# Kernel optimization log

Measured on AMD Instinct MI355X. Metric: run time of the kernel, lower is better.

The kernel has to match this reference:

```python
import jax, jax.numpy as jnp
import numpy as np

LP, LQ, B, D = 4096, 4096, 32, 512  # lp, lq, batch, hidden (=in_size1=in_size2)
WSCALE = 0.04  # ~ torch Linear default uniform bound 1/sqrt(512)


def setup_inputs() -> dict:
    key = jax.random.key(0)
    ks = jax.random.split(key, 11)
    return {
        "h": jax.random.normal(ks[0], (LP, B, D), jnp.float32),
        "u": jax.random.normal(ks[1], (B, LQ, D), jnp.float32),
        "v": jax.random.normal(ks[2], (B, D, 1), jnp.float32),
        "Wu_w": jax.random.normal(ks[3], (D, D), jnp.float32) * WSCALE,
        "Wu_b": jax.random.normal(ks[4], (D,), jnp.float32) * WSCALE,
        "Wh_w": jax.random.normal(ks[5], (D, D), jnp.float32) * WSCALE,
        "Wha_w": jax.random.normal(ks[6], (D, D), jnp.float32) * WSCALE,
        "W_ih": jax.random.normal(ks[7], (3 * D, D), jnp.float32) * WSCALE,
        "W_hh": jax.random.normal(ks[8], (3 * D, D), jnp.float32) * WSCALE,
        "b_ih": jax.random.normal(ks[9], (3 * D,), jnp.float32) * WSCALE,
        "b_hh": jax.random.normal(ks[10], (3 * D,), jnp.float32) * WSCALE,
    }


def _gru_cell(x, hprev, W_ih, W_hh, b_ih, b_hh):
    # torch GRUCell semantics
    gi = x @ W_ih.T + b_ih          # [B, 3D]
    gh = hprev @ W_hh.T + b_hh      # [B, 3D]
    i_r, i_z, i_n = jnp.split(gi, 3, axis=-1)
    h_r, h_z, h_n = jnp.split(gh, 3, axis=-1)
    r = jax.nn.sigmoid(i_r + h_r)
    z = jax.nn.sigmoid(i_z + h_z)
    n = jnp.tanh(i_n + r * h_n)
    return (1.0 - z) * n + z * hprev


def reference(h, u, v, Wu_w, Wu_b, Wh_w, Wha_w, W_ih, W_hh, b_ih, b_hh):
    # h: [lp, B, d1], u: [B, lq, d2], v: [B, H, 1]
    vb = v[:, :, 0]  # [B, H]
    # --- attention over u ---
    xq = jnp.tanh(jnp.einsum('bqd,hd->bqh', u, Wu_w) + Wu_b)   # [B, lq, H]
    s = jnp.einsum('bqh,bh->bq', xq, vb)                        # bmm(x, v).squeeze
    a = jax.nn.softmax(s, axis=1)
    r = jnp.einsum('bq,bqd->bd', a, u)                          # [B, d2]
    # --- attention over h conditioned on r, twice with GRU update in between ---
    Whh_proj = jnp.einsum('pbd,hd->pbh', h, Wh_w)               # [lp, B, H] (reused)

    def h_attn(rvec):
        x = jnp.tanh(Whh_proj + (rvec @ Wha_w.T)[None])         # [lp, B, H]
        s = jnp.einsum('pbh,bh->bp', x, vb)                     # [B, lp]
        return jax.nn.softmax(s, axis=1)

    p1 = h_attn(r)
    c = jnp.einsum('bp,pbd->bd', p1, h)                         # [B, d1]
    r2 = _gru_cell(c, r, W_ih, W_hh, b_ih, b_hh)                # [B, d2]
    p2 = h_attn(r2)
    return (p1, p2)
```

## Files before the change

kernel.cpp:

```cpp
#include <hip/hip_runtime.h>
#include <hip/hip_bf16.h>

typedef __attribute__((ext_vector_type(4))) float f4;
typedef __attribute__((ext_vector_type(8))) _Float16 h8;
typedef __attribute__((ext_vector_type(4))) _Float16 h4;

#define MTOT 131072

__device__ __forceinline__ float fast_tanh(float x){
    float e = exp2f(x * 2.8853900817779268f);
    return 1.0f - 2.0f * __builtin_amdgcn_rcpf(e + 1.0f);
}
__device__ __forceinline__ float fast_sigmoid(float x){
    return __builtin_amdgcn_rcpf(1.0f + exp2f(-x * 1.4426950408889634f));
}
__device__ __forceinline__ float wave_reduce_sum(float v){
    #pragma unroll
    for (int off = 32; off; off >>= 1) v += __shfl_down(v, off, 64);
    return v;
}

__device__ __forceinline__ void gl_lds16(const void* g, void* l){
    __builtin_amdgcn_global_load_lds(
        (const __attribute__((address_space(1))) void*)g,
        (__attribute__((address_space(3))) void*)l, 16, 0, 0);
}

__global__ __launch_bounds__(256) void k_pack_w(const float* __restrict__ W, _Float16* __restrict__ Wp){
    const int idx = blockIdx.x * 4 + (threadIdx.x >> 6);
    const int l = threadIdx.x & 63;
    const int n = (idx >> 4) * 16 + (l & 15);
    const int k = (idx & 15) * 32 + (l >> 4) * 8;
    const float* src = W + n * 512 + k;
    f4 s0 = *(const f4*)(src);
    f4 s1 = *(const f4*)(src + 4);
    h8 v;
    #pragma unroll
    for (int i = 0; i < 4; i++){ v[i] = (_Float16)s0[i]; v[4+i] = (_Float16)s1[i]; }
    *(h8*)(Wp + (idx << 9) + l * 8) = v;
}

union SMem {
    struct { float A[2][4096]; _Float16 W[2][8192]; } st;
    _Float16 ep[64][264];
};

template<int MODE>
__global__ __launch_bounds__(512) void k_score_gemm(
    const float* __restrict__ A,
    const _Float16* __restrict__ Wp,
    const float* __restrict__ vb,
    const float* __restrict__ addvec,
    float* __restrict__ spart,
    _Float16* __restrict__ whh)
{
    __shared__ __align__(16) SMem sm;

    const int tid  = threadIdx.x;
    const int lane = tid & 63;
    const int wv   = tid >> 6;
    const int wr   = wv >> 2;
    const int wc   = wv & 3;
    const int mt   = blockIdx.x >> 1;
    const int nc   = blockIdx.x & 1;
    const int m0   = mt * 128;
    const int n0   = nc * 256;

    const int lr = lane & 15;
    const int kq = lane >> 4;

    const int arow0 = tid >> 3;
    const int aseg  = tid & 7;

    auto stage = [&](int kt, int buf){
        #pragma unroll
        for (int i = 0; i < 2; i++){
            const int row = arow0 + i*64;
            const int sg  = aseg ^ (row & 7);
            const float* g = A + (long)(m0 + row)*512 + kt*32 + sg*4;
            char* l = (char*)&sm.st.A[0][0] + buf*16384 + (i*512 + wv*64)*16;
            gl_lds16(g, l);
        }
        #pragma unroll
        for (int i = 0; i < 2; i++){
            const int chunk = i*8 + wv;
            const _Float16* g = Wp + ((long)((nc*16 + chunk)*16 + kt))*512 + lane*8;
            char* l = (char*)&sm.st.W[0][0] + buf*16384 + chunk*1024;
            gl_lds16(g, l);
        }
    };

    f4 acc[4][4] = {};

    stage(0, 0);
    __syncthreads();

    const int plo = (2*kq)     ^ (lr & 7);
    const int phi = (2*kq + 1) ^ (lr & 7);

    for (int kt = 0; kt < 16; ++kt){
        const int buf = kt & 1;
        if (kt < 15) stage(kt + 1, buf ^ 1);

        const float* Ab = &sm.st.A[0][0] + buf*4096;
        h8 af[4];
        #pragma unroll
        for (int mi = 0; mi < 4; mi++){
            const int row = wr*64 + mi*16 + lr;
            f4 lo = *(const f4*)(Ab + row*32 + plo*4);
            f4 hi = *(const f4*)(Ab + row*32 + phi*4);
            h8 v;
            #pragma unroll
            for (int i = 0; i < 4; i++){ v[i] = (_Float16)lo[i]; v[4+i] = (_Float16)hi[i]; }
            af[mi] = v;
        }
        const _Float16* Wb = &sm.st.W[0][0] + buf*8192;
        h8 bf[4];
        #pragma unroll
        for (int ni = 0; ni < 4; ni++)
            bf[ni] = *(const h8*)(Wb + (wc*4 + ni)*512 + lane*8);

        #pragma unroll
        for (int mi = 0; mi < 4; mi++)
            #pragma unroll
            for (int ni = 0; ni < 4; ni++)
                acc[mi][ni] = __builtin_amdgcn_mfma_f32_16x16x32_f16(af[mi], bf[ni], acc[mi][ni], 0, 0, 0);

        __syncthreads();
    }

    const int jrow = (lane >> 4) * 4;
    for (int hf = 0; hf < 2; ++hf){
        if (wr == hf){
            #pragma unroll
            for (int mi = 0; mi < 4; mi++)
                #pragma unroll
                for (int ni = 0; ni < 4; ni++)
                    #pragma unroll
                    for (int j = 0; j < 4; j++)
                        sm.ep[mi*16 + jrow + j][wc*64 + ni*16 + lr] = (_Float16)acc[mi][ni][j];
        }
        __syncthreads();

        if (MODE == 1 && whh){
            const int row = tid >> 3, seg = tid & 7;
            const int m = m0 + hf*64 + row;
            const _Float16* esrc = &sm.ep[row][seg*32];
            _Float16* gdst = whh + (long)m*512 + n0 + seg*32;
            #pragma unroll
            for (int i = 0; i < 4; i++)
                *(h8*)(gdst + i*8) = *(const h8*)(esrc + i*8);
        }

        #pragma unroll
        for (int rr = 0; rr < 8; ++rr){
            const int erow = wv*8 + rr;
            const int m = m0 + hf*64 + erow;
            const int b = (MODE == 0) ? (m >> 12) : (m & 31);
            const int n = n0 + lane*4;
            h4 hv = *(const h4*)&sm.ep[erow][lane*4];
            f4 vbv = *(const f4*)&vb[b*512 + n];
            f4 adv;
            if (MODE == 0) adv = *(const f4*)&addvec[n];
            else           adv = *(const f4*)&addvec[b*512 + n];
            float p = 0.f;
            #pragma unroll
            for (int i = 0; i < 4; i++)
                p += fast_tanh((float)hv[i] + adv[i]) * vbv[i];
            p = wave_reduce_sum(p);
            if (lane == 0){
                const int sIdx = (MODE == 0) ? m : (((m & 31) << 12) | (m >> 5));
                spart[nc*MTOT + sIdx] = p;
            }
        }
        __syncthreads();
    }
}

__global__ __launch_bounds__(256) void k_softmax(const float* __restrict__ s0,
        const float* __restrict__ s1, float* __restrict__ out)
{
    __shared__ float red[8];
    __shared__ float bcast[2];
    const int b = blockIdx.x, t = threadIdx.x;
    const int wv = t >> 6, lane = t & 63;
    const float* p0 = s0 + b*4096;
    const float* p1 = s1 ? s1 + b*4096 : nullptr;
    float vals[16];
    float mx = -3.0e38f;
    #pragma unroll
    for (int i = 0; i < 16; i++){
        float v = p0[t + i*256];
        if (p1) v += p1[t + i*256];
        vals[i] = v;
        mx = fmaxf(mx, v);
    }
    #pragma unroll
    for (int off = 32; off; off >>= 1) mx = fmaxf(mx, __shfl_down(mx, off, 64));
    if (lane == 0) red[wv] = mx;
    __syncthreads();
    if (t == 0) bcast[0] = fmaxf(fmaxf(red[0], red[1]), fmaxf(red[2], red[3]));
    __syncthreads();
    const float gmax = bcast[0];
    float sum = 0.f;
    #pragma unroll
    for (int i = 0; i < 16; i++){
        vals[i] = exp2f((vals[i] - gmax) * 1.4426950408889634f);
        sum += vals[i];
    }
    sum = wave_reduce_sum(sum);
    if (lane == 0) red[wv] = sum;
    __syncthreads();
    if (t == 0) bcast[1] = red[0] + red[1] + red[2] + red[3];
    __syncthreads();
    const float inv = 1.0f / bcast[1];
    #pragma unroll
    for (int i = 0; i < 16; i++) out[b*4096 + t + i*256] = vals[i] * inv;
}

__global__ __launch_bounds__(512) void k_weighted_rowsum(
    const float* __restrict__ wts, const float* __restrict__ X,
    float* __restrict__ part, int mode)
{
    const int b = blockIdx.x, ch = blockIdx.y, d = threadIdx.x;
    float acc = 0.f;
    const int q0 = ch * 256;
    for (int q = q0; q < q0 + 256; ++q){
        const float w = wts[b*4096 + q];
        if (fabsf(w) > 1e-20f){
            const float* xp = (mode == 0) ? (X + ((long)(b*4096 + q) * 512) + d)
                                          : (X + ((long)(q*32 + b) * 512) + d);
            acc += w * xp[0];
        }
    }
    part[(ch*32 + b)*512 + d] = acc;
}

__global__ void k_reduce_part(const float* __restrict__ part, float* __restrict__ out){
    const int b = blockIdx.x, d = threadIdx.x;
    float s = 0.f;
    #pragma unroll
    for (int ch = 0; ch < 16; ++ch) s += part[(ch*32 + b)*512 + d];
    out[b*512 + d] = s;
}

__global__ __launch_bounds__(256) void k_matvec(
    const float* __restrict__ W, const float* __restrict__ x,
    const float* __restrict__ bias, float* __restrict__ out, int N)
{
    __shared__ float xs[512];
    const int b = blockIdx.x, t = threadIdx.x;
    xs[t] = x[b*512 + t];
    xs[t + 256] = x[b*512 + 256 + t];
    __syncthreads();
    const int wv = t >> 6, lane = t & 63;
    const int rbase = blockIdx.y*32 + wv*8;
    for (int rr = 0; rr < 8; ++rr){
        const int row = rbase + rr;
        const float* wp = W + (long)row*512;
        float p = 0.f;
        #pragma unroll
        for (int j = 0; j < 8; j++) p += wp[lane + j*64] * xs[lane + j*64];
        p = wave_reduce_sum(p);
        if (lane == 0) out[b*N + row] = p + (bias ? bias[row] : 0.f);
    }
}

__global__ void k_gru(const float* __restrict__ gi, const float* __restrict__ gh,
                      const float* __restrict__ r, float* __restrict__ r2)
{
    const int b = blockIdx.x, d = threadIdx.x;
    const float* gib = gi + b*1536;
    const float* ghb = gh + b*1536;
    const float rg = fast_sigmoid(gib[d]        + ghb[d]);
    const float z  = fast_sigmoid(gib[512 + d]  + ghb[512 + d]);
    const float n  = fast_tanh   (gib[1024 + d] + rg * ghb[1024 + d]);
    r2[b*512 + d] = (1.f - z)*n + z*r[b*512 + d];
}

__global__ __launch_bounds__(256) void k_t2(const _Float16* __restrict__ whh,
        const float* __restrict__ vb, const float* __restrict__ ra2, float* __restrict__ t2)
{
    const int wv = threadIdx.x >> 6, lane = threadIdx.x & 63;
    const int mbase = blockIdx.x*32 + wv*8;
    for (int rr = 0; rr < 8; ++rr){
        const int m = mbase + rr;
        const int b = m & 31;
        h8 hv = *(const h8*)(whh + (long)m*512 + lane*8);
        const float* rp  = ra2 + b*512 + lane*8;
        const float* vbp = vb  + b*512 + lane*8;
        float p = 0.f;
        #pragma unroll
        for (int i = 0; i < 8; i++)
            p += fast_tanh((float)hv[i] + rp[i]) * vbp[i];
        p = wave_reduce_sum(p);
        if (lane == 0) t2[((m & 31) << 12) | (m >> 5)] = p;
    }
}

extern "C" void kernel_launch(void* const* d_in, const int* in_sizes, int n_in,
                              void* d_out, int out_size, void* d_ws, size_t ws_size,
                              hipStream_t stream)
{
    const float* h_    = (const float*)d_in[0];
    const float* u_    = (const float*)d_in[1];
    const float* vb    = (const float*)d_in[2];
    const float* Wu_w  = (const float*)d_in[3];
    const float* Wu_b  = (const float*)d_in[4];
    const float* Wh_w  = (const float*)d_in[5];
    const float* Wha_w = (const float*)d_in[6];
    const float* W_ih  = (const float*)d_in[7];
    const float* W_hh  = (const float*)d_in[8];
    const float* b_ih  = (const float*)d_in[9];
    const float* b_hh  = (const float*)d_in[10];
    float* out = (float*)d_out;

    char* ws = (char*)d_ws;
    float*    spart = (float*)(ws + 0);
    float*    tpart = (float*)(ws + 1048576);
    float*    a_    = (float*)(ws + 2097152);
    _Float16* Wpu   = (_Float16*)(ws + 2621440);
    _Float16* Wph   = (_Float16*)(ws + 3145728);
    float*    r_    = (float*)(ws + 3670016);
    float*    ra1   = (float*)(ws + 3735552);
    float*    c_    = (float*)(ws + 3801088);
    float*    r2    = (float*)(ws + 3866624);
    float*    ra2   = (float*)(ws + 3932160);
    float*    gi    = (float*)(ws + 3997696);
    float*    gh    = (float*)(ws + 4194304);
    float*    rpart = (float*)(ws + 4390912);
    float*    cpart = (float*)(ws + 5439488);
    _Float16* whh   = (_Float16*)(ws + 8388608);
    const bool big = ws_size >= (size_t)8388608 + (size_t)MTOT * 512 * 2;

    k_pack_w<<<128, 256, 0, stream>>>(Wu_w, Wpu);
    k_pack_w<<<128, 256, 0, stream>>>(Wh_w, Wph);

    k_score_gemm<0><<<2048, 512, 0, stream>>>(u_, Wpu, vb, Wu_b, spart, nullptr);
    k_softmax<<<32, 256, 0, stream>>>(spart, spart + MTOT, a_);
    k_weighted_rowsum<<<dim3(32, 16), 512, 0, stream>>>(a_, u_, rpart, 0);
    k_reduce_part<<<32, 512, 0, stream>>>(rpart, r_);
    k_matvec<<<dim3(32, 16), 256, 0, stream>>>(Wha_w, r_, nullptr, ra1, 512);

    k_score_gemm<1><<<2048, 512, 0, stream>>>(h_, Wph, vb, ra1, tpart, big ? whh : nullptr);
    k_softmax<<<32, 256, 0, stream>>>(tpart, tpart + MTOT, out);

    k_weighted_rowsum<<<dim3(32, 16), 512, 0, stream>>>(out, h_, cpart, 1);
    k_reduce_part<<<32, 512, 0, stream>>>(cpart, c_);
    k_matvec<<<dim3(32, 48), 256, 0, stream>>>(W_ih, c_, b_ih, gi, 1536);
    k_matvec<<<dim3(32, 48), 256, 0, stream>>>(W_hh, r_, b_hh, gh, 1536);
    k_gru<<<32, 512, 0, stream>>>(gi, gh, r_, r2);
    k_matvec<<<dim3(32, 16), 256, 0, stream>>>(Wha_w, r2, nullptr, ra2, 512);

    if (big){
        k_t2<<<4096, 256, 0, stream>>>(whh, vb, ra2, tpart);
        k_softmax<<<32, 256, 0, stream>>>(tpart, nullptr, out + MTOT);
    } else {
        k_score_gemm<2><<<2048, 512, 0, stream>>>(h_, Wph, vb, ra2, tpart, nullptr);
        k_softmax<<<32, 256, 0, stream>>>(tpart, tpart + MTOT, out + MTOT);
    }
}
```

Baseline: 598.8 us.

## Triple-buffer score GEMM and fuse softmax/rowsum/matvec/GRU tails into per-batch kernels

The score GEMM moves from a double-buffered to a triple-buffered global-to-LDS pipeline. It uses explicit vmcnt waits, raw barriers and raised MFMA priority, so loads for step kt+3 overlap compute. The softmax, weighted rowsum, partial reduce, matvec and GRU kernels are replaced by two fused kernels with one block per batch. Each builds a sparse list of non-negligible weights and does the rowsum and matvecs in-block, and the two weight-pack launches are merged into one. This cuts about ten launches and intermediate buffers, but the rowsum and matvecs now run on only 32 blocks, which could underuse the GPU.

Measured after the change: 919.6 us. 1.54x slower.

```diff
diff --git a/kernel.cpp b/kernel.cpp
--- a/kernel.cpp
+++ b/kernel.cpp
@@ -26,8 +26,14 @@
         (__attribute__((address_space(3))) void*)l, 16, 0, 0);
 }
 
-__global__ __launch_bounds__(256) void k_pack_w(const float* __restrict__ W, _Float16* __restrict__ Wp){
-    const int idx = blockIdx.x * 4 + (threadIdx.x >> 6);
+__global__ __launch_bounds__(256) void k_pack_both(
+    const float* __restrict__ Wu, const float* __restrict__ Wh,
+    _Float16* __restrict__ Pu, _Float16* __restrict__ Ph)
+{
+    const int g = blockIdx.x;
+    const float* W = (g < 128) ? Wu : Wh;
+    _Float16*    P = (g < 128) ? Pu : Ph;
+    const int idx = (g & 127) * 4 + (threadIdx.x >> 6);
     const int l = threadIdx.x & 63;
     const int n = (idx >> 4) * 16 + (l & 15);
     const int k = (idx & 15) * 32 + (l >> 4) * 8;
@@ -37,11 +43,11 @@
     h8 v;
     #pragma unroll
     for (int i = 0; i < 4; i++){ v[i] = (_Float16)s0[i]; v[4+i] = (_Float16)s1[i]; }
-    *(h8*)(Wp + (idx << 9) + l * 8) = v;
+    *(h8*)(P + (idx << 9) + l * 8) = v;
 }
 
 union SMem {
-    struct { float A[2][4096]; _Float16 W[2][8192]; } st;
+    struct { float A[3][4096]; _Float16 W[3][8192]; } st;
     _Float16 ep[64][264];
 };
 
@@ -92,15 +98,20 @@
 
     f4 acc[4][4] = {};
 
-    stage(0, 0);
-    __syncthreads();
+    stage(0, 0); stage(1, 1); stage(2, 2);
+    __builtin_amdgcn_sched_barrier(0);
 
     const int plo = (2*kq)     ^ (lr & 7);
     const int phi = (2*kq + 1) ^ (lr & 7);
 
+    #pragma unroll
     for (int kt = 0; kt < 16; ++kt){
-        const int buf = kt & 1;
-        if (kt < 15) stage(kt + 1, buf ^ 1);
+        const int buf = kt % 3;
+        if (kt < 14)       asm volatile("s_waitcnt vmcnt(8)" ::: "memory");
+        else if (kt == 14) asm volatile("s_waitcnt vmcnt(4)" ::: "memory");
+        else               asm volatile("s_waitcnt vmcnt(0)" ::: "memory");
+        __builtin_amdgcn_s_barrier();
+        __builtin_amdgcn_sched_barrier(0);
 
         const float* Ab = &sm.st.A[0][0] + buf*4096;
         h8 af[4];
@@ -120,14 +131,23 @@
         for (int ni = 0; ni < 4; ni++)
             bf[ni] = *(const h8*)(Wb + (wc*4 + ni)*512 + lane*8);
 
+        asm volatile("s_waitcnt lgkmcnt(0)" ::: "memory");
+        __builtin_amdgcn_sched_barrier(0);
+        __builtin_amdgcn_s_barrier();
+        __builtin_amdgcn_sched_barrier(0);
+
+        if (kt < 13) stage(kt + 3, buf);
+
+        __builtin_amdgcn_s_setprio(1);
         #pragma unroll
         for (int mi = 0; mi < 4; mi++)
             #pragma unroll
             for (int ni = 0; ni < 4; ni++)
                 acc[mi][ni] = __builtin_amdgcn_mfma_f32_16x16x32_f16(af[mi], bf[ni], acc[mi][ni], 0, 0, 0);
-
-        __syncthreads();
-    }
+        __builtin_amdgcn_s_setprio(0);
+    }
+    __builtin_amdgcn_sched_barrier(0);
+    __syncthreads();
 
     const int jrow = (lane >> 4) * 4;
     for (int hf = 0; hf < 2; ++hf){
@@ -177,6 +197,163 @@
     }
 }
 
+__global__ __launch_bounds__(512) void k_fused1(
+    const float* __restrict__ sp, const float* __restrict__ u,
+    const float* __restrict__ Wha,
+    float* __restrict__ r_out, float* __restrict__ ra1)
+{
+    __shared__ float aw[4096];
+    __shared__ int   qlist[4096];
+    __shared__ float xl[512];
+    __shared__ float red[8];
+    __shared__ float bc[2];
+    __shared__ int   cnt;
+    const int b = blockIdx.x, t = threadIdx.x;
+    const int wv = t >> 6, lane = t & 63;
+    if (t == 0) cnt = 0;
+    const float* p0 = sp + b*4096;
+    const float* p1 = sp + MTOT + b*4096;
+    float v[8]; float mx = -3.0e38f;
+    #pragma unroll
+    for (int i = 0; i < 8; i++){
+        v[i] = p0[t + i*512] + p1[t + i*512];
+        mx = fmaxf(mx, v[i]);
+    }
+    #pragma unroll
+    for (int off = 32; off; off >>= 1) mx = fmaxf(mx, __shfl_down(mx, off, 64));
+    if (lane == 0) red[wv] = mx;
+    __syncthreads();
+    if (t == 0){ float m2 = red[0]; for (int i = 1; i < 8; i++) m2 = fmaxf(m2, red[i]); bc[0] = m2; }
+    __syncthreads();
+    const float gmax = bc[0];
+    float sum = 0.f;
+    #pragma unroll
+    for (int i = 0; i < 8; i++){
+        float e = exp2f((v[i] - gmax) * 1.4426950408889634f);
+        v[i] = e; aw[t + i*512] = e; sum += e;
+        if (e > 1e-16f){ int idx = atomicAdd(&cnt, 1); qlist[idx] = t + i*512; }
+    }
+    sum = wave_reduce_sum(sum);
+    if (lane == 0) red[wv] = sum;
+    __syncthreads();
+    if (t == 0){ float s2 = 0.f; for (int i = 0; i < 8; i++) s2 += red[i]; bc[1] = s2; }
+    __syncthreads();
+    const float inv = 1.0f / bc[1];
+    const int n = cnt;
+    float acc = 0.f;
+    for (int i = 0; i < n; i++){
+        const int q = qlist[i];
+        acc += aw[q] * u[((long)(b*4096 + q))*512 + t];
+    }
+    acc *= inv;
+    xl[t] = acc;
+    r_out[b*512 + t] = acc;
+    __syncthreads();
+    for (int j = 0; j < 64; j++){
+        const int row = wv*64 + j;
+        const float* wp = Wha + (long)row*512;
+        float p = 0.f;
+        #pragma unroll
+        for (int jj = 0; jj < 8; jj++) p += wp[lane + jj*64] * xl[lane + jj*64];
+        p = wave_reduce_sum(p);
+        if (lane == 0) ra1[b*512 + row] = p;
+    }
+}
+
+__global__ __launch_bounds__(512) void k_fused2(
+    const float* __restrict__ tp, const float* __restrict__ h,
+    const float* __restrict__ r_in,
+    const float* __restrict__ Wih, const float* __restrict__ Whh_,
+    const float* __restrict__ bih, const float* __restrict__ bhh,
+    const float* __restrict__ Wha,
+    float* __restrict__ p1_out, float* __restrict__ ra2)
+{
+    __shared__ float aw[4096];
+    __shared__ int   qlist[4096];
+    __shared__ float cl[512], rl[512], r2l[512];
+    __shared__ float gl[1536], hl[1536];
+    __shared__ float red[8];
+    __shared__ float bc[2];
+    __shared__ int   cnt;
+    const int b = blockIdx.x, t = threadIdx.x;
+    const int wv = t >> 6, lane = t & 63;
+    if (t == 0) cnt = 0;
+    rl[t] = r_in[b*512 + t];
+    const float* p0 = tp + b*4096;
+    const float* p1 = tp + MTOT + b*4096;
+    float v[8]; float mx = -3.0e38f;
+    #pragma unroll
+    for (int i = 0; i < 8; i++){
+        v[i] = p0[t + i*512] + p1[t + i*512];
+        mx = fmaxf(mx, v[i]);
+    }
+    #pragma unroll
+    for (int off = 32; off; off >>= 1) mx = fmaxf(mx, __shfl_down(mx, off, 64));
+    if (lane == 0) red[wv] = mx;
+    __syncthreads();
+    if (t == 0){ float m2 = red[0]; for (int i = 1; i < 8; i++) m2 = fmaxf(m2, red[i]); bc[0] = m2; }
+    __syncthreads();
+    const float gmax = bc[0];
+    float sum = 0.f;
+    #pragma unroll
+    for (int i = 0; i < 8; i++){
+        float e = exp2f((v[i] - gmax) * 1.4426950408889634f);
+        v[i] = e; aw[t + i*512] = e; sum += e;
+        if (e > 1e-16f){ int idx = atomicAdd(&cnt, 1); qlist[idx] = t + i*512; }
+    }
+    sum = wave_reduce_sum(sum);
+    if (lane == 0) red[wv] = sum;
+    __syncthreads();
+    if (t == 0){ float s2 = 0.f; for (int i = 0; i < 8; i++) s2 += red[i]; bc[1] = s2; }
+    __syncthreads();
+    const float inv = 1.0f / bc[1];
+    const int n = cnt;
+    #pragma unroll
+    for (int i = 0; i < 8; i++) p1_out[b*4096 + t + i*512] = v[i] * inv;
+    float acc = 0.f;
+    for (int i = 0; i < n; i++){
+        const int q = qlist[i];
+        acc += aw[q] * h[((long)(q*32 + b))*512 + t];
+    }
+    cl[t] = acc * inv;
+    __syncthreads();
+    for (int j = 0; j < 192; j++){
+        const int row = wv*192 + j;
+        const float* wp = Wih + (long)row*512;
+        float p = 0.f;
+        #pragma unroll
+        for (int jj = 0; jj < 8; jj++) p += wp[lane + jj*64] * cl[lane + jj*64];
+        p = wave_reduce_sum(p);
+        if (lane == 0) gl[row] = p + bih[row];
+    }
+    for (int j = 0; j < 192; j++){
+        const int row = wv*192 + j;
+        const float* wp = Whh_ + (long)row*512;
+        float p = 0.f;
+        #pragma unroll
+        for (int jj = 0; jj < 8; jj++) p += wp[lane + jj*64] * rl[lane + jj*64];
+        p = wave_reduce_sum(p);
+        if (lane == 0) hl[row] = p + bhh[row];
+    }
+    __syncthreads();
+    {
+        const float rg = fast_sigmoid(gl[t] + hl[t]);
+        const float z  = fast_sigmoid(gl[512 + t] + hl[512 + t]);
+        const float nn = fast_tanh(gl[1024 + t] + rg * hl[1024 + t]);
+        r2l[t] = (1.f - z)*nn + z*rl[t];
+    }
+    __syncthreads();
+    for (int j = 0; j < 64; j++){
+        const int row = wv*64 + j;
+        const float* wp = Wha + (long)row*512;
+        float p = 0.f;
+        #pragma unroll
+        for (int jj = 0; jj < 8; jj++) p += wp[lane + jj*64] * r2l[lane + jj*64];
+        p = wave_reduce_sum(p);
+        if (lane == 0) ra2[b*512 + row] = p;
+    }
+}
+
 __global__ __launch_bounds__(256) void k_softmax(const float* __restrict__ s0,
         const float* __restrict__ s1, float* __restrict__ out)
 {
@@ -216,66 +393,6 @@
     const float inv = 1.0f / bcast[1];
     #pragma unroll
     for (int i = 0; i < 16; i++) out[b*4096 + t + i*256] = vals[i] * inv;
-}
-
-__global__ __launch_bounds__(512) void k_weighted_rowsum(
-    const float* __restrict__ wts, const float* __restrict__ X,
-    float* __restrict__ part, int mode)
-{
-    const int b = blockIdx.x, ch = blockIdx.y, d = threadIdx.x;
-    float acc = 0.f;
-    const int q0 = ch * 256;
-    for (int q = q0; q < q0 + 256; ++q){
-        const float w = wts[b*4096 + q];
-        if (fabsf(w) > 1e-20f){
-            const float* xp = (mode == 0) ? (X + ((long)(b*4096 + q) * 512) + d)
-                                          : (X + ((long)(q*32 + b) * 512) + d);
-            acc += w * xp[0];
-        }
-    }
-    part[(ch*32 + b)*512 + d] = acc;
-}
-
-__global__ void k_reduce_part(const float* __restrict__ part, float* __restrict__ out){
-    const int b = blockIdx.x, d = threadIdx.x;
-    float s = 0.f;
-    #pragma unroll
-    for (int ch = 0; ch < 16; ++ch) s += part[(ch*32 + b)*512 + d];
-    out[b*512 + d] = s;
-}
-
-__global__ __launch_bounds__(256) void k_matvec(
-    const float* __restrict__ W, const float* __restrict__ x,
-    const float* __restrict__ bias, float* __restrict__ out, int N)
-{
-    __shared__ float xs[512];
-    const int b = blockIdx.x, t = threadIdx.x;
-    xs[t] = x[b*512 + t];
-    xs[t + 256] = x[b*512 + 256 + t];
-    __syncthreads();
-    const int wv = t >> 6, lane = t & 63;
-    const int rbase = blockIdx.y*32 + wv*8;
-    for (int rr = 0; rr < 8; ++rr){
-        const int row = rbase + rr;
-        const float* wp = W + (long)row*512;
-        float p = 0.f;
-        #pragma unroll
-        for (int j = 0; j < 8; j++) p += wp[lane + j*64] * xs[lane + j*64];
-        p = wave_reduce_sum(p);
-        if (lane == 0) out[b*N + row] = p + (bias ? bias[row] : 0.f);
-    }
-}
-
-__global__ void k_gru(const float* __restrict__ gi, const float* __restrict__ gh,
-                      const float* __restrict__ r, float* __restrict__ r2)
-{
-    const int b = blockIdx.x, d = threadIdx.x;
-    const float* gib = gi + b*1536;
-    const float* ghb = gh + b*1536;
-    const float rg = fast_sigmoid(gib[d]        + ghb[d]);
-    const float z  = fast_sigmoid(gib[512 + d]  + ghb[512 + d]);
-    const float n  = fast_tanh   (gib[1024 + d] + rg * ghb[1024 + d]);
-    r2[b*512 + d] = (1.f - z)*n + z*r[b*512 + d];
 }
 
 __global__ __launch_bounds__(256) void k_t2(const _Float16* __restrict__ whh,
@@ -318,39 +435,21 @@
     char* ws = (char*)d_ws;
     float*    spart = (float*)(ws + 0);
     float*    tpart = (float*)(ws + 1048576);
-    float*    a_    = (float*)(ws + 2097152);
     _Float16* Wpu   = (_Float16*)(ws + 2621440);
     _Float16* Wph   = (_Float16*)(ws + 3145728);
     float*    r_    = (float*)(ws + 3670016);
     float*    ra1   = (float*)(ws + 3735552);
-    float*    c_    = (float*)(ws + 3801088);
-    float*    r2    = (float*)(ws + 3866624);
     float*    ra2   = (float*)(ws + 3932160);
-    float*    gi    = (float*)(ws + 3997696);
-    float*    gh    = (float*)(ws + 4194304);
-    float*    rpart = (float*)(ws + 4390912);
-    float*    cpart = (float*)(ws + 5439488);
     _Float16* whh   = (_Float16*)(ws + 8388608);
     const bool big = ws_size >= (size_t)8388608 + (size_t)MTOT * 512 * 2;
 
-    k_pack_w<<<128, 256, 0, stream>>>(Wu_w, Wpu);
-    k_pack_w<<<128, 256, 0, stream>>>(Wh_w, Wph);
+    k_pack_both<<<256, 256, 0, stream>>>(Wu_w, Wh_w, Wpu, Wph);
 
     k_score_gemm<0><<<2048, 512, 0, stream>>>(u_, Wpu, vb, Wu_b, spart, nullptr);
-    k_softmax<<<32, 256, 0, stream>>>(spart, spart + MTOT, a_);
-    k_weighted_rowsum<<<dim3(32, 16), 512, 0, stream>>>(a_, u_, rpart, 0);
-    k_reduce_part<<<32, 512, 0, stream>>>(rpart, r_);
-    k_matvec<<<dim3(32, 16), 256, 0, stream>>>(Wha_w, r_, nullptr, ra1, 512);
+    k_fused1<<<32, 512, 0, stream>>>(spart, u_, Wha_w, r_, ra1);
 
     k_score_gemm<1><<<2048, 512, 0, stream>>>(h_, Wph, vb, ra1, tpart, big ? whh : nullptr);
-    k_softmax<<<32, 256, 0, stream>>>(tpart, tpart + MTOT, out);
-
-    k_weighted_rowsum<<<dim3(32, 16), 512, 0, stream>>>(out, h_, cpart, 1);
-    k_reduce_part<<<32, 512, 0, stream>>>(cpart, c_);
-    k_matvec<<<dim3(32, 48), 256, 0, stream>>>(W_ih, c_, b_ih, gi, 1536);
-    k_matvec<<<dim3(32, 48), 256, 0, stream>>>(W_hh, r_, b_hh, gh, 1536);
-    k_gru<<<32, 512, 0, stream>>>(gi, gh, r_, r2);
-    k_matvec<<<dim3(32, 16), 256, 0, stream>>>(Wha_w, r2, nullptr, ra2, 512);
+    k_fused2<<<32, 512, 0, stream>>>(tpart, h_, r_, W_ih, W_hh, b_ih, b_hh, Wha_w, out, ra2);
 
     if (big){
         k_t2<<<4096, 256, 0, stream>>>(whh, vb, ra2, tpart);
```

## Triple-buffer score GEMM pipeline, merge weight packing, widen rowsum split, vectorize matvec

Applied to the files above, without the earlier changes.

The score GEMM moves from a double-buffered to a triple-buffered LDS pipeline. It waits with explicit vmcnt and uses raw barriers, setprio around the MFMAs, and a fully unrolled k loop, so global loads for the stage after next overlap compute. The two weight-pack launches are merged into one, and the weighted row-sum is split into 32 chunks instead of 16 for more parallelism, with one shared partial buffer. The matvec now uses contiguous float4 loads per lane. The larger LDS footprint may lower occupancy, and the partial buffer grows to 2 MB in the workspace.

Result: no change. 593.0 us (-1.0%).

```diff
diff --git a/kernel.cpp b/kernel.cpp
--- a/kernel.cpp
+++ b/kernel.cpp
@@ -26,8 +26,14 @@
         (__attribute__((address_space(3))) void*)l, 16, 0, 0);
 }
 
-__global__ __launch_bounds__(256) void k_pack_w(const float* __restrict__ W, _Float16* __restrict__ Wp){
-    const int idx = blockIdx.x * 4 + (threadIdx.x >> 6);
+__global__ __launch_bounds__(256) void k_pack_both(
+    const float* __restrict__ Wu, const float* __restrict__ Wh,
+    _Float16* __restrict__ Pu, _Float16* __restrict__ Ph)
+{
+    const int g = blockIdx.x;
+    const float* W = (g < 128) ? Wu : Wh;
+    _Float16*    P = (g < 128) ? Pu : Ph;
+    const int idx = (g & 127) * 4 + (threadIdx.x >> 6);
     const int l = threadIdx.x & 63;
     const int n = (idx >> 4) * 16 + (l & 15);
     const int k = (idx & 15) * 32 + (l >> 4) * 8;
@@ -37,11 +43,11 @@
     h8 v;
     #pragma unroll
     for (int i = 0; i < 4; i++){ v[i] = (_Float16)s0[i]; v[4+i] = (_Float16)s1[i]; }
-    *(h8*)(Wp + (idx << 9) + l * 8) = v;
+    *(h8*)(P + (idx << 9) + l * 8) = v;
 }
 
 union SMem {
-    struct { float A[2][4096]; _Float16 W[2][8192]; } st;
+    struct { float A[3][4096]; _Float16 W[3][8192]; } st;
     _Float16 ep[64][264];
 };
 
@@ -92,15 +98,20 @@
 
     f4 acc[4][4] = {};
 
-    stage(0, 0);
-    __syncthreads();
+    stage(0, 0); stage(1, 1); stage(2, 2);
+    __builtin_amdgcn_sched_barrier(0);
 
     const int plo = (2*kq)     ^ (lr & 7);
     const int phi = (2*kq + 1) ^ (lr & 7);
 
+    #pragma unroll
     for (int kt = 0; kt < 16; ++kt){
-        const int buf = kt & 1;
-        if (kt < 15) stage(kt + 1, buf ^ 1);
+        const int buf = kt % 3;
+        if (kt < 14)       asm volatile("s_waitcnt vmcnt(8)" ::: "memory");
+        else if (kt == 14) asm volatile("s_waitcnt vmcnt(4)" ::: "memory");
+        else               asm volatile("s_waitcnt vmcnt(0)" ::: "memory");
+        __builtin_amdgcn_s_barrier();
+        __builtin_amdgcn_sched_barrier(0);
 
         const float* Ab = &sm.st.A[0][0] + buf*4096;
         h8 af[4];
@@ -120,14 +131,23 @@
         for (int ni = 0; ni < 4; ni++)
             bf[ni] = *(const h8*)(Wb + (wc*4 + ni)*512 + lane*8);
 
+        asm volatile("s_waitcnt lgkmcnt(0)" ::: "memory");
+        __builtin_amdgcn_sched_barrier(0);
+        __builtin_amdgcn_s_barrier();
+        __builtin_amdgcn_sched_barrier(0);
+
+        if (kt < 13) stage(kt + 3, buf);
+
+        __builtin_amdgcn_s_setprio(1);
         #pragma unroll
         for (int mi = 0; mi < 4; mi++)
             #pragma unroll
             for (int ni = 0; ni < 4; ni++)
                 acc[mi][ni] = __builtin_amdgcn_mfma_f32_16x16x32_f16(af[mi], bf[ni], acc[mi][ni], 0, 0, 0);
-
-        __syncthreads();
-    }
+        __builtin_amdgcn_s_setprio(0);
+    }
+    __builtin_amdgcn_sched_barrier(0);
+    __syncthreads();
 
     const int jrow = (lane >> 4) * 4;
     for (int hf = 0; hf < 2; ++hf){
@@ -224,8 +244,8 @@
 {
     const int b = blockIdx.x, ch = blockIdx.y, d = threadIdx.x;
     float acc = 0.f;
-    const int q0 = ch * 256;
-    for (int q = q0; q < q0 + 256; ++q){
+    const int q0 = ch * 128;
+    for (int q = q0; q < q0 + 128; ++q){
         const float w = wts[b*4096 + q];
         if (fabsf(w) > 1e-20f){
             const float* xp = (mode == 0) ? (X + ((long)(b*4096 + q) * 512) + d)
@@ -240,7 +260,7 @@
     const int b = blockIdx.x, d = threadIdx.x;
     float s = 0.f;
     #pragma unroll
-    for (int ch = 0; ch < 16; ++ch) s += part[(ch*32 + b)*512 + d];
+    for (int ch = 0; ch < 32; ++ch) s += part[(ch*32 + b)*512 + d];
     out[b*512 + d] = s;
 }
 
@@ -254,13 +274,16 @@
     xs[t + 256] = x[b*512 + 256 + t];
     __syncthreads();
     const int wv = t >> 6, lane = t & 63;
+    f4 x0 = *(const f4*)&xs[lane*8];
+    f4 x1 = *(const f4*)&xs[lane*8 + 4];
     const int rbase = blockIdx.y*32 + wv*8;
     for (int rr = 0; rr < 8; ++rr){
         const int row = rbase + rr;
-        const float* wp = W + (long)row*512;
-        float p = 0.f;
-        #pragma unroll
-        for (int j = 0; j < 8; j++) p += wp[lane + j*64] * xs[lane + j*64];
+        const float* wp = W + (long)row*512 + lane*8;
+        f4 w0 = *(const f4*)wp;
+        f4 w1 = *(const f4*)(wp + 4);
+        float p = w0[0]*x0[0] + w0[1]*x0[1] + w0[2]*x0[2] + w0[3]*x0[3]
+                + w1[0]*x1[0] + w1[1]*x1[1] + w1[2]*x1[2] + w1[3]*x1[3];
         p = wave_reduce_sum(p);
         if (lane == 0) out[b*N + row] = p + (bias ? bias[row] : 0.f);
     }
@@ -328,25 +351,23 @@
     float*    ra2   = (float*)(ws + 3932160);
     float*    gi    = (float*)(ws + 3997696);
     float*    gh    = (float*)(ws + 4194304);
-    float*    rpart = (float*)(ws + 4390912);
-    float*    cpart = (float*)(ws + 5439488);
+    float*    part  = (float*)(ws + 4390912);
     _Float16* whh   = (_Float16*)(ws + 8388608);
     const bool big = ws_size >= (size_t)8388608 + (size_t)MTOT * 512 * 2;
 
-    k_pack_w<<<128, 256, 0, stream>>>(Wu_w, Wpu);
-    k_pack_w<<<128, 256, 0, stream>>>(Wh_w, Wph);
+    k_pack_both<<<256, 256, 0, stream>>>(Wu_w, Wh_w, Wpu, Wph);
 
     k_score_gemm<0><<<2048, 512, 0, stream>>>(u_, Wpu, vb, Wu_b, spart, nullptr);
     k_softmax<<<32, 256, 0, stream>>>(spart, spart + MTOT, a_);
-    k_weighted_rowsum<<<dim3(32, 16), 512, 0, stream>>>(a_, u_, rpart, 0);
-    k_reduce_part<<<32, 512, 0, stream>>>(rpart, r_);
+    k_weighted_rowsum<<<dim3(32, 32), 512, 0, stream>>>(a_, u_, part, 0);
+    k_reduce_part<<<32, 512, 0, stream>>>(part, r_);
     k_matvec<<<dim3(32, 16), 256, 0, stream>>>(Wha_w, r_, nullptr, ra1, 512);
 
     k_score_gemm<1><<<2048, 512, 0, stream>>>(h_, Wph, vb, ra1, tpart, big ? whh : nullptr);
     k_softmax<<<32, 256, 0, stream>>>(tpart, tpart + MTOT, out);
 
-    k_weighted_rowsum<<<dim3(32, 16), 512, 0, stream>>>(out, h_, cpart, 1);
-    k_reduce_part<<<32, 512, 0, stream>>>(cpart, c_);
+    k_weighted_rowsum<<<dim3(32, 32), 512, 0, stream>>>(out, h_, part, 1);
+    k_reduce_part<<<32, 512, 0, stream>>>(part, c_);
     k_matvec<<<dim3(32, 48), 256, 0, stream>>>(W_ih, c_, b_ih, gi, 1536);
     k_matvec<<<dim3(32, 48), 256, 0, stream>>>(W_hh, r_, b_hh, gh, 1536);
     k_gru<<<32, 512, 0, stream>>>(gi, gh, r_, r2);
```
